# Performance work log

Hardware: AMD Instinct MI355X
Metric: run time of the kernel (lower is better)

The kernel has to match this reference:

```python
import jax, jax.numpy as jnp
import numpy as np

N0, N1, N2 = 16000, 12000, 6000
K0, K1 = 10, 5
H, OUT = 256, 128
VOCABS = [50000, 1000, 200]
EDIMS = [64, 32, 32]
EIN = sum(EDIMS)  # 128 input to fc_input


def setup_inputs() -> dict:
    key = jax.random.key(0)
    ks = jax.random.split(key, 40)
    inp = {}
    cols = [jax.random.randint(ks[i], (N0, 1), 0, VOCABS[i]) for i in range(3)]
    inp['x'] = jnp.concatenate(cols, axis=1)
    inp['idx_sim0'] = jax.random.randint(ks[3], (N1, K0), 0, N0)
    inp['idx_cor0'] = jax.random.randint(ks[4], (N1, K0), 0, N0)
    inp['idx_sim1'] = jax.random.randint(ks[5], (N2, K1), 0, N1)
    inp['idx_cor1'] = jax.random.randint(ks[6], (N2, K1), 0, N1)
    k = 7
    for m in ['sim', 'cor']:
        for i in range(3):
            inp[f'emb{i}_{m}'] = jax.random.normal(ks[k], (VOCABS[i], EDIMS[i]), jnp.float32) * 0.02; k += 1
        inp[f'Win_{m}'] = jax.random.normal(ks[k], (EIN, H), jnp.float32) * (1.0 / np.sqrt(EIN)); k += 1
        inp[f'bin_{m}'] = jnp.zeros((H,), jnp.float32)
        inp[f'Wout_{m}'] = jax.random.normal(ks[k], (H, OUT), jnp.float32) * (1.0 / np.sqrt(H)); k += 1
        inp[f'bout_{m}'] = jnp.zeros((OUT,), jnp.float32)
    inp['Ws2c'] = jax.random.normal(ks[k], (OUT, OUT), jnp.float32) * (1.0 / np.sqrt(OUT)); k += 1
    inp['Wc2s'] = jax.random.normal(ks[k], (OUT, OUT), jnp.float32) * (1.0 / np.sqrt(OUT)); k += 1
    inp['a1'] = jnp.array([0.3], jnp.float32)
    inp['a2'] = jnp.array([0.25], jnp.float32)
    inp['b2'] = jnp.array([0.2], jnp.float32)
    return inp


def _coattention(D, Q):
    # D, Q: [N, K, H]
    L = jnp.einsum('nkh,nmh->nkm', D, Q)          # [N, K, K]
    AC = jax.nn.softmax(L, axis=-1)
    AS = jax.nn.softmax(jnp.swapaxes(L, 1, 2), axis=-1)
    CQ = jnp.einsum('nkm,nmh->nkh', AC, Q)        # [N, K, H]
    CD = jnp.einsum('nkm,nmh->nkh', AS, jnp.concatenate([D, CQ], axis=-1))  # [N, K, 2H]
    return jnp.concatenate([Q, CD], axis=-1)       # [N, K, 3H]


def _coagg(feat, idx_sim, idx_cor, mode, n_dst):
    # gather neighbor features per dst node (feat_src[in_edges_id])
    if mode == 'cor':
        D, Q = feat[idx_sim], feat[idx_cor]
    else:
        D, Q = feat[idx_cor], feat[idx_sim]
    h = _coattention(D, Q)                         # [n_dst, K, 3H]
    n, k, f = h.shape
    # AvgPool1d(kernel=3, stride=3) over feature axis -> [n_dst, K, H]
    pooled = h.reshape(n, k, f // 3, 3).mean(axis=-1)
    neigh = pooled.mean(axis=1)                    # mean over neighbors -> [n_dst, H]
    return feat[:n_dst] + neigh


def _branch(x, e0, e1, e2, Win, bin_, Wout, bout, i_s0, i_c0, i_s1, i_c1, mode):
    e = jnp.concatenate([e0[x[:, 0]], e1[x[:, 1]], e2[x[:, 2]]], axis=1)  # [N0, 128]
    h = e @ Win + bin_                             # [N0, H]
    h = jax.nn.relu(_coagg(h, i_s0, i_c0, mode, N1))
    h = _coagg(h, i_s1, i_c1, mode, N2)
    return h @ Wout + bout                         # [N2, OUT]


def reference(x, idx_sim0, idx_cor0, idx_sim1, idx_cor1,
              emb0_sim, emb1_sim, emb2_sim, Win_sim, bin_sim, Wout_sim, bout_sim,
              emb0_cor, emb1_cor, emb2_cor, Win_cor, bin_cor, Wout_cor, bout_cor,
              Ws2c, Wc2s, a1, a2, b2):
    sim = _branch(x, emb0_sim, emb1_sim, emb2_sim, Win_sim, bin_sim, Wout_sim, bout_sim,
                  idx_sim0, idx_cor0, idx_sim1, idx_cor1, 'sim')
    cor = _branch(x, emb0_cor, emb1_cor, emb2_cor, Win_cor, bin_cor, Wout_cor, bout_cor,
                  idx_sim0, idx_cor0, idx_sim1, idx_cor1, 'cor')
    # SemanticIntegration
    z1sim = (1 - a1) * sim + a1 * (cor @ Wc2s)
    z1cor = (1 - a1) * cor + a1 * (sim @ Ws2c)
    z2sim = (1 - a2 - b2) * sim + a2 * (cor @ Wc2s) + b2 * (z1cor @ Wc2s)
    z2cor = (1 - a2 - b2) * cor + a2 * (sim @ Ws2c) + b2 * (z1sim @ Ws2c)
    return jnp.stack([z2sim, z2cor])               # [2, N2, OUT]
```

## Files before the change

kernel.cpp:

```cpp
#include <hip/hip_runtime.h>

#define CH 256

template <int CTRL>
__device__ __forceinline__ float dppAdd(float v) {
    const int m = __builtin_amdgcn_update_dpp(0, __builtin_bit_cast(int, v), CTRL, 0xf, 0xf, true);
    return v + __builtin_bit_cast(float, m);
}

#define OPAQUE4(v) asm volatile("" : "+v"((v).x), "+v"((v).y), "+v"((v).z), "+v"((v).w))

__device__ __forceinline__ unsigned short f2bf(float f) {
    unsigned int x = __builtin_bit_cast(unsigned int, f);
    return (unsigned short)((x + 0x7fffu + ((x >> 16) & 1u)) >> 16);
}
__device__ __forceinline__ float bf2f(unsigned short u) {
    return __builtin_bit_cast(float, ((unsigned int)u) << 16);
}

__global__ __launch_bounds__(256) void embed_fc2_kernel(
    const int* __restrict__ x,
    const float* __restrict__ e0a, const float* __restrict__ e1a, const float* __restrict__ e2a,
    const float* __restrict__ Wina, const float* __restrict__ bina, unsigned short* __restrict__ h0a,
    const float* __restrict__ e0b, const float* __restrict__ e1b, const float* __restrict__ e2b,
    const float* __restrict__ Winb, const float* __restrict__ binb, unsigned short* __restrict__ h0b,
    const int blocksPer)
{
    __shared__ __align__(16) float eT[128][32];
    int bid = blockIdx.x;
    const float *e0, *e1, *e2, *Win, *bin;
    unsigned short* h0;
    if (bid < blocksPer) { e0 = e0a; e1 = e1a; e2 = e2a; Win = Wina; bin = bina; h0 = h0a; }
    else { bid -= blocksPer; e0 = e0b; e1 = e1b; e2 = e2b; Win = Winb; bin = binb; h0 = h0b; }

    const int row0 = bid * 32;
    const int t = threadIdx.x;
    const int w = t >> 6, l = t & 63;
    const int r = l & 31;
    const int kcBase = 2 * w + (l >> 5);

#pragma unroll
    for (int j = 0; j < 4; ++j) {
        const int kc = kcBase + 8 * j;
        const int k0 = kc * 4;
        const int row = row0 + r;
        float4 v;
        if (kc < 16)      v = *(const float4*)(e0 + (size_t)x[row * 3 + 0] * 64 + k0);
        else if (kc < 24) v = *(const float4*)(e1 + (size_t)x[row * 3 + 1] * 32 + (k0 - 64));
        else              v = *(const float4*)(e2 + (size_t)x[row * 3 + 2] * 32 + (k0 - 96));
        eT[k0 + 0][r] = v.x; eT[k0 + 1][r] = v.y; eT[k0 + 2][r] = v.z; eT[k0 + 3][r] = v.w;
    }
    __syncthreads();

    const float4 bb = *(const float4*)(bin + l * 4);
    float acc[8][4];
#pragma unroll
    for (int rr = 0; rr < 8; ++rr) {
        acc[rr][0] = bb.x; acc[rr][1] = bb.y; acc[rr][2] = bb.z; acc[rr][3] = bb.w;
    }
#pragma unroll 4
    for (int k = 0; k < 128; ++k) {
        const float4 wv = *(const float4*)(Win + (size_t)k * 256 + l * 4);
        const float4 ea = *(const float4*)&eT[k][w * 8];
        const float4 eb = *(const float4*)&eT[k][w * 8 + 4];
        const float ev[8] = {ea.x, ea.y, ea.z, ea.w, eb.x, eb.y, eb.z, eb.w};
#pragma unroll
        for (int rr = 0; rr < 8; ++rr) {
            acc[rr][0] += ev[rr] * wv.x; acc[rr][1] += ev[rr] * wv.y;
            acc[rr][2] += ev[rr] * wv.z; acc[rr][3] += ev[rr] * wv.w;
        }
    }
#pragma unroll
    for (int rr = 0; rr < 8; ++rr) {
        ushort4 o;
        o.x = f2bf(acc[rr][0]); o.y = f2bf(acc[rr][1]);
        o.z = f2bf(acc[rr][2]); o.w = f2bf(acc[rr][3]);
        *(ushort4*)(h0 + (size_t)(row0 + w * 8 + rr) * 256 + l * 4) = o;
    }
}

template <int KD, int MODE>
__global__ __launch_bounds__(128) void gemm16_kernel(
    const float* __restrict__ ina, const float* __restrict__ Wa,
    const float* __restrict__ auxa, const float* __restrict__ aux2a, float* __restrict__ oa,
    const float* __restrict__ inb, const float* __restrict__ Wb,
    const float* __restrict__ auxb, const float* __restrict__ aux2b, float* __restrict__ ob,
    const int blocksPer, const int nRows,
    const float* __restrict__ a1p, const float* __restrict__ a2p, const float* __restrict__ b2p)
{
    __shared__ __align__(16) float inT[KD][16];
    int bid = blockIdx.x;
    const float *in, *W, *aux, *aux2; float* outp;
    if (bid < blocksPer) { in = ina; W = Wa; aux = auxa; aux2 = aux2a; outp = oa; }
    else { bid -= blocksPer; in = inb; W = Wb; aux = auxb; aux2 = aux2b; outp = ob; }

    const int row0 = bid * 16;
    const int t = threadIdx.x;
    const int row = t & 15;
    const int kc0 = t >> 4;

#pragma unroll
    for (int j = 0; j < KD / 32; ++j) {
        const int kc = kc0 + 8 * j;
        const int k0 = kc * 4;
        int r = row0 + row;
        if (r >= nRows) r = nRows - 1;
        const float4 v = *(const float4*)(in + (size_t)r * KD + k0);
        inT[k0 + 0][row] = v.x; inT[k0 + 1][row] = v.y;
        inT[k0 + 2][row] = v.z; inT[k0 + 3][row] = v.w;
    }
    __syncthreads();

    const int w = t >> 6, l = t & 63;
    const int rg = w * 2 + (l >> 5);
    const int r0 = rg * 4;
    const int cc0 = (l & 31) * 4;

    float acc[4][4];
    if constexpr (MODE == 0) {
        const float4 bb = *(const float4*)(aux + cc0);
#pragma unroll
        for (int rr = 0; rr < 4; ++rr) {
            acc[rr][0] = bb.x; acc[rr][1] = bb.y; acc[rr][2] = bb.z; acc[rr][3] = bb.w;
        }
    } else {
#pragma unroll
        for (int rr = 0; rr < 4; ++rr) acc[rr][0] = acc[rr][1] = acc[rr][2] = acc[rr][3] = 0.f;
    }

#pragma unroll 4
    for (int k = 0; k < KD; ++k) {
        const float4 wv = *(const float4*)(W + (size_t)k * 128 + cc0);
        const float4 ea = *(const float4*)&inT[k][r0];
        const float ev[4] = {ea.x, ea.y, ea.z, ea.w};
#pragma unroll
        for (int rr = 0; rr < 4; ++rr) {
            acc[rr][0] += ev[rr] * wv.x; acc[rr][1] += ev[rr] * wv.y;
            acc[rr][2] += ev[rr] * wv.z; acc[rr][3] += ev[rr] * wv.w;
        }
    }

    float c0 = 0.f, c1 = 0.f, c2 = 0.f;
    if constexpr (MODE == 1) {
        const float a1 = *a1p, a2 = *a2p, b2 = *b2p;
        c0 = 1.f - a2 - b2;
        c1 = a2 + b2 * (1.f - a1);
        c2 = b2 * a1;
    }

#pragma unroll
    for (int rr = 0; rr < 4; ++rr) {
        const int r = row0 + r0 + rr;
        if (r < nRows) {
            float4 o = make_float4(acc[rr][0], acc[rr][1], acc[rr][2], acc[rr][3]);
            if constexpr (MODE == 1) {
                const size_t idx = (size_t)r * 128 + cc0;
                const float4 b1v = *(const float4*)(aux + idx);
                const float4 b2v = *(const float4*)(aux2 + idx);
                o.x = c0 * b1v.x + c1 * b2v.x + c2 * o.x;
                o.y = c0 * b1v.y + c1 * b2v.y + c2 * o.y;
                o.z = c0 * b1v.z + c1 * b2v.z + c2 * o.z;
                o.w = c0 * b1v.w + c1 * b2v.w + c2 * o.w;
            }
            *(float4*)(outp + (size_t)r * 128 + cc0) = o;
        }
    }
}

template <int K, bool BF16IN>
__global__ __launch_bounds__(256, 2) void coagg_kernel(
    const void* __restrict__ fa, const int* __restrict__ iDa, const int* __restrict__ iQa,
    float* __restrict__ oa,
    const void* __restrict__ fb, const int* __restrict__ iDb, const int* __restrict__ iQb,
    float* __restrict__ ob,
    const int nPer, const int relu)
{
    __shared__ float sL[4][K][K];
    __shared__ float sAC[4][K][K];
    __shared__ float sAS[4][K][K];
    __shared__ float sw_[4][K], su_[4][K];
    __shared__ __align__(16) float sHsum[4][768];

    const int t = threadIdx.x;
    const int wv = t >> 6, lane = t & 63;
    int n = blockIdx.x * 4 + wv;

    const void* feat; const int* idxD; const int* idxQ; float* outp;
    if (n < nPer) { feat = fa; idxD = iDa; idxQ = iQa; outp = oa; }
    else { n -= nPer; feat = fb; idxD = iDb; idxQ = iQb; outp = ob; }

    float4 d[K], q[K], resid;
    if constexpr (BF16IN) {
        const unsigned short* fpu = (const unsigned short*)feat;
#pragma unroll
        for (int k = 0; k < K; ++k) {
            const int rD = idxD[n * K + k];
            const int rQ = idxQ[n * K + k];
            const ushort4 ud = *(const ushort4*)(fpu + (size_t)rD * 256 + lane * 4);
            const ushort4 uq = *(const ushort4*)(fpu + (size_t)rQ * 256 + lane * 4);
            d[k] = make_float4(bf2f(ud.x), bf2f(ud.y), bf2f(ud.z), bf2f(ud.w));
            q[k] = make_float4(bf2f(uq.x), bf2f(uq.y), bf2f(uq.z), bf2f(uq.w));
        }
        const ushort4 ur = *(const ushort4*)(fpu + (size_t)n * 256 + lane * 4);
        resid = make_float4(bf2f(ur.x), bf2f(ur.y), bf2f(ur.z), bf2f(ur.w));
    } else {
        const float4* fp = (const float4*)feat;
#pragma unroll
        for (int k = 0; k < K; ++k) {
            const int rD = idxD[n * K + k];
            const int rQ = idxQ[n * K + k];
            d[k] = fp[(size_t)rD * 64 + lane];
            q[k] = fp[(size_t)rQ * 64 + lane];
        }
        resid = fp[(size_t)n * 64 + lane];
    }
#pragma unroll
    for (int k = 0; k < K; ++k) { OPAQUE4(d[k]); OPAQUE4(q[k]); }

#pragma unroll
    for (int k = 0; k < K; ++k) {
        const float4 dd = d[k];
#pragma unroll
        for (int m0 = 0; m0 < K; m0 += 4) {
            const float4 q0 = q[m0];
            float s0 = dd.x * q0.x + dd.y * q0.y + dd.z * q0.z + dd.w * q0.w;
            float s1 = 0.f, s2 = 0.f, s3 = 0.f;
            if (m0 + 1 < K) {
                const float4 qq = q[(m0 + 1 < K) ? m0 + 1 : 0];
                s1 = dd.x * qq.x + dd.y * qq.y + dd.z * qq.z + dd.w * qq.w;
            }
            if (m0 + 2 < K) {
                const float4 qq = q[(m0 + 2 < K) ? m0 + 2 : 0];
                s2 = dd.x * qq.x + dd.y * qq.y + dd.z * qq.z + dd.w * qq.w;
            }
            if (m0 + 3 < K) {
                const float4 qq = q[(m0 + 3 < K) ? m0 + 3 : 0];
                s3 = dd.x * qq.x + dd.y * qq.y + dd.z * qq.z + dd.w * qq.w;
            }
            asm volatile("v_permlane32_swap_b32 %0, %1" : "+v"(s0), "+v"(s1));
            float a = s0 + s1;
            asm volatile("v_permlane32_swap_b32 %0, %1" : "+v"(s2), "+v"(s3));
            float b = s2 + s3;
            asm volatile("v_permlane16_swap_b32 %0, %1" : "+v"(a), "+v"(b));
            float r = a + b;
            r = dppAdd<0x111>(r);
            r = dppAdd<0x112>(r);
            r = dppAdd<0x114>(r);
            r = dppAdd<0x118>(r);
            const int rowid = lane >> 4;
            const int mm = m0 + (((rowid & 1) << 1) | (rowid >> 1));
            if ((lane & 15) == 15 && mm < K) sL[wv][k][mm] = r;
        }
    }

    if (lane < K) {
        float e_[K], mx = -1e30f;
#pragma unroll
        for (int m = 0; m < K; ++m) mx = fmaxf(mx, sL[wv][lane][m]);
        float ssum = 0.f;
#pragma unroll
        for (int m = 0; m < K; ++m) { e_[m] = __expf(sL[wv][lane][m] - mx); ssum += e_[m]; }
        const float inv = 1.f / ssum;
#pragma unroll
        for (int m = 0; m < K; ++m) sAC[wv][lane][m] = e_[m] * inv;
    }
    {
        const int c = lane - 16;
        if (c >= 0 && c < K) {
            float e_[K], mx = -1e30f;
#pragma unroll
            for (int m = 0; m < K; ++m) mx = fmaxf(mx, sL[wv][m][c]);
            float ssum = 0.f;
#pragma unroll
            for (int m = 0; m < K; ++m) { e_[m] = __expf(sL[wv][m][c] - mx); ssum += e_[m]; }
            const float inv = 1.f / ssum;
#pragma unroll
            for (int m = 0; m < K; ++m) sAS[wv][c][m] = e_[m] * inv;
        }
    }
    {
        const int m2 = lane - 32;
        if (m2 >= 0 && m2 < K) {
            float s = 0.f;
#pragma unroll
            for (int k2 = 0; k2 < K; ++k2) s += sAS[wv][k2][m2];
            sw_[wv][m2] = s;
        }
    }
    {
        const int j2 = lane - 48;
        if (j2 >= 0 && j2 < K) {
            float s = 0.f;
#pragma unroll
            for (int m = 0; m < K; ++m) s += sw_[wv][m] * sAC[wv][m][j2];
            su_[wv][j2] = s;
        }
    }

    float4 h0v = make_float4(0.f, 0.f, 0.f, 0.f);
    float4 h1v = make_float4(0.f, 0.f, 0.f, 0.f);
    float4 h2v = make_float4(0.f, 0.f, 0.f, 0.f);
#pragma unroll
    for (int kx = 0; kx < K; ++kx) {
        const float wk = sw_[wv][kx];
        const float uk = su_[wv][kx];
        const float4 qq = q[kx];
        const float4 dd = d[kx];
        h0v.x += qq.x;      h0v.y += qq.y;      h0v.z += qq.z;      h0v.w += qq.w;
        h1v.x += wk * dd.x; h1v.y += wk * dd.y; h1v.z += wk * dd.z; h1v.w += wk * dd.w;
        h2v.x += uk * qq.x; h2v.y += uk * qq.y; h2v.z += uk * qq.z; h2v.w += uk * qq.w;
    }
    ((float4*)&sHsum[wv][0])[lane]       = h0v;
    ((float4*)&sHsum[wv][0])[64 + lane]  = h1v;
    ((float4*)&sHsum[wv][0])[128 + lane] = h2v;

    float ov[4];
#pragma unroll
    for (int i = 0; i < 4; ++i) {
        const int f = lane * 4 + i;
        ov[i] = (sHsum[wv][3 * f] + sHsum[wv][3 * f + 1] + sHsum[wv][3 * f + 2])
                * (1.0f / (3.0f * K));
    }
    float4 o = make_float4(resid.x + ov[0], resid.y + ov[1],
                           resid.z + ov[2], resid.w + ov[3]);
    if (relu) {
        o.x = fmaxf(o.x, 0.f); o.y = fmaxf(o.y, 0.f);
        o.z = fmaxf(o.z, 0.f); o.w = fmaxf(o.w, 0.f);
    }
    ((float4*)outp)[(size_t)n * 64 + lane] = o;
}

extern "C" void kernel_launch(void* const* d_in, const int* in_sizes, int n_in,
                              void* d_out, int out_size, void* d_ws, size_t ws_size,
                              hipStream_t stream)
{
    const int* x        = (const int*)d_in[0];
    const int* idx_sim0 = (const int*)d_in[1];
    const int* idx_cor0 = (const int*)d_in[2];
    const int* idx_sim1 = (const int*)d_in[3];
    const int* idx_cor1 = (const int*)d_in[4];
    const float* e0s  = (const float*)d_in[5];
    const float* e1s  = (const float*)d_in[6];
    const float* e2s  = (const float*)d_in[7];
    const float* Wins = (const float*)d_in[8];
    const float* bins = (const float*)d_in[9];
    const float* Wouts= (const float*)d_in[10];
    const float* bouts= (const float*)d_in[11];
    const float* e0c  = (const float*)d_in[12];
    const float* e1c  = (const float*)d_in[13];
    const float* e2c  = (const float*)d_in[14];
    const float* Winc = (const float*)d_in[15];
    const float* binc = (const float*)d_in[16];
    const float* Woutc= (const float*)d_in[17];
    const float* boutc= (const float*)d_in[18];
    const float* Ws2c = (const float*)d_in[19];
    const float* Wc2s = (const float*)d_in[20];
    const float* a1 = (const float*)d_in[21];
    const float* a2 = (const float*)d_in[22];
    const float* b2 = (const float*)d_in[23];

    float* outSim = (float*)d_out;
    float* outCor = outSim + 6000 * 128;

    float* ws = (float*)d_ws;
    const size_t needMerged = (size_t)(2 * 16000 * 256 + 2 * 12000 * 256 + 2 * 6000 * 256 + 4 * 6000 * 128) * 4;
    const bool merged = ws_size >= needMerged;

    const int fcBlocks = 6000 / 16;

    if (merged) {
        unsigned short* A0 = (unsigned short*)ws;
        unsigned short* A1 = (unsigned short*)(ws + 16000 * 256);
        float* B0 = ws + 2 * 16000 * 256;
        float* B1 = B0 + 12000 * 256;
        float* C0 = B1 + 12000 * 256;
        float* C1 = C0 + 6000 * 256;
        float* simO = C1 + 6000 * 256;
        float* corO = simO + 6000 * 128;
        float* P    = corO + 6000 * 128;
        float* S    = P + 6000 * 128;

        embed_fc2_kernel<<<1000, 256, 0, stream>>>(x,
            e0s, e1s, e2s, Wins, bins, A0,
            e0c, e1c, e2c, Winc, binc, A1, 500);
        coagg_kernel<10, true><<<6000, 256, 0, stream>>>(
            A0, idx_cor0, idx_sim0, B0,
            A1, idx_sim0, idx_cor0, B1, 12000, 1);
        coagg_kernel<5, false><<<3000, 256, 0, stream>>>(
            B0, idx_cor1, idx_sim1, C0,
            B1, idx_sim1, idx_cor1, C1, 6000, 0);
        gemm16_kernel<256, 0><<<2 * fcBlocks, 128, 0, stream>>>(
            C0, Wouts, bouts, nullptr, simO,
            C1, Woutc, boutc, nullptr, corO, fcBlocks, 6000, a1, a2, b2);
        gemm16_kernel<128, 2><<<2 * fcBlocks, 128, 0, stream>>>(
            corO, Wc2s, nullptr, nullptr, P,
            simO, Ws2c, nullptr, nullptr, S, fcBlocks, 6000, a1, a2, b2);
        gemm16_kernel<128, 1><<<2 * fcBlocks, 128, 0, stream>>>(
            S, Wc2s, simO, P, outSim,
            P, Ws2c, corO, S, outCor, fcBlocks, 6000, a1, a2, b2);
    } else {
        unsigned short* A = (unsigned short*)ws;
        float* B = ws + 16000 * 256;
        float* C = B + 12000 * 256;
        float* simO = C + 6000 * 256;
        float* corO = simO + 6000 * 128;
        float* P    = corO + 6000 * 128;
        float* S    = P + 6000 * 128;

        for (int b = 0; b < 2; ++b) {
            const float* e0   = (b == 0) ? e0s : e0c;
            const float* e1   = (b == 0) ? e1s : e1c;
            const float* e2   = (b == 0) ? e2s : e2c;
            const float* Win  = (b == 0) ? Wins : Winc;
            const float* bin  = (b == 0) ? bins : binc;
            const float* Wout = (b == 0) ? Wouts : Woutc;
            const float* bout = (b == 0) ? bouts : boutc;
            const int* iD0 = (b == 0) ? idx_cor0 : idx_sim0;
            const int* iQ0 = (b == 0) ? idx_sim0 : idx_cor0;
            const int* iD1 = (b == 0) ? idx_cor1 : idx_sim1;
            const int* iQ1 = (b == 0) ? idx_sim1 : idx_cor1;
            float* branchOut = (b == 0) ? simO : corO;

            embed_fc2_kernel<<<500, 256, 0, stream>>>(x,
                e0, e1, e2, Win, bin, A,
                e0, e1, e2, Win, bin, A, 500);
            coagg_kernel<10, true><<<3000, 256, 0, stream>>>(
                A, iD0, iQ0, B, A, iD0, iQ0, B, 12000, 1);
            coagg_kernel<5, false><<<1500, 256, 0, stream>>>(
                B, iD1, iQ1, C, B, iD1, iQ1, C, 6000, 0);
            gemm16_kernel<256, 0><<<fcBlocks, 128, 0, stream>>>(
                C, Wout, bout, nullptr, branchOut,
                C, Wout, bout, nullptr, branchOut, fcBlocks, 6000, a1, a2, b2);
        }
        gemm16_kernel<128, 2><<<2 * fcBlocks, 128, 0, stream>>>(
            corO, Wc2s, nullptr, nullptr, P,
            simO, Ws2c, nullptr, nullptr, S, fcBlocks, 6000, a1, a2, b2);
        gemm16_kernel<128, 1><<<2 * fcBlocks, 128, 0, stream>>>(
            S, Wc2s, simO, P, outSim,
            P, Ws2c, corO, S, outCor, fcBlocks, 6000, a1, a2, b2);
    }
}
```

Before: 157.2 us.

## Store layer-1 coagg output in bf16 and fuse integration GEMMs into one kernel

The first coattention layer now writes its intermediate features as bf16, and the second layer reads them as bf16. This halves the bytes moved through the gather-heavy second stage. The two semantic-integration GEMM launches are merged into one kernel that keeps the intermediate S/P products in shared memory, which removes one launch and a global round trip. In exchange, the layer-1 output loses precision, and the fused kernel uses small 8-row tiles that reread the weight matrices many times.

```diff
diff --git a/kernel.cpp b/kernel.cpp
--- a/kernel.cpp
+++ b/kernel.cpp
@@ -79,20 +79,18 @@
     }
 }
 
-template <int KD, int MODE>
-__global__ __launch_bounds__(128) void gemm16_kernel(
+__global__ __launch_bounds__(128) void fcout_kernel(
     const float* __restrict__ ina, const float* __restrict__ Wa,
-    const float* __restrict__ auxa, const float* __restrict__ aux2a, float* __restrict__ oa,
+    const float* __restrict__ auxa, float* __restrict__ oa,
     const float* __restrict__ inb, const float* __restrict__ Wb,
-    const float* __restrict__ auxb, const float* __restrict__ aux2b, float* __restrict__ ob,
-    const int blocksPer, const int nRows,
-    const float* __restrict__ a1p, const float* __restrict__ a2p, const float* __restrict__ b2p)
+    const float* __restrict__ auxb, float* __restrict__ ob,
+    const int blocksPer, const int nRows)
 {
-    __shared__ __align__(16) float inT[KD][16];
+    __shared__ __align__(16) float inT[256][16];
     int bid = blockIdx.x;
-    const float *in, *W, *aux, *aux2; float* outp;
-    if (bid < blocksPer) { in = ina; W = Wa; aux = auxa; aux2 = aux2a; outp = oa; }
-    else { bid -= blocksPer; in = inb; W = Wb; aux = auxb; aux2 = aux2b; outp = ob; }
+    const float *in, *W, *aux; float* outp;
+    if (bid < blocksPer) { in = ina; W = Wa; aux = auxa; outp = oa; }
+    else { bid -= blocksPer; in = inb; W = Wb; aux = auxb; outp = ob; }
 
     const int row0 = bid * 16;
     const int t = threadIdx.x;
@@ -100,12 +98,12 @@
     const int kc0 = t >> 4;
 
 #pragma unroll
-    for (int j = 0; j < KD / 32; ++j) {
+    for (int j = 0; j < 8; ++j) {
         const int kc = kc0 + 8 * j;
         const int k0 = kc * 4;
         int r = row0 + row;
         if (r >= nRows) r = nRows - 1;
-        const float4 v = *(const float4*)(in + (size_t)r * KD + k0);
+        const float4 v = *(const float4*)(in + (size_t)r * 256 + k0);
         inT[k0 + 0][row] = v.x; inT[k0 + 1][row] = v.y;
         inT[k0 + 2][row] = v.z; inT[k0 + 3][row] = v.w;
     }
@@ -117,19 +115,14 @@
     const int cc0 = (l & 31) * 4;
 
     float acc[4][4];
-    if constexpr (MODE == 0) {
-        const float4 bb = *(const float4*)(aux + cc0);
-#pragma unroll
-        for (int rr = 0; rr < 4; ++rr) {
-            acc[rr][0] = bb.x; acc[rr][1] = bb.y; acc[rr][2] = bb.z; acc[rr][3] = bb.w;
-        }
-    } else {
-#pragma unroll
-        for (int rr = 0; rr < 4; ++rr) acc[rr][0] = acc[rr][1] = acc[rr][2] = acc[rr][3] = 0.f;
+    const float4 bb = *(const float4*)(aux + cc0);
+#pragma unroll
+    for (int rr = 0; rr < 4; ++rr) {
+        acc[rr][0] = bb.x; acc[rr][1] = bb.y; acc[rr][2] = bb.z; acc[rr][3] = bb.w;
     }
 
 #pragma unroll 4
-    for (int k = 0; k < KD; ++k) {
+    for (int k = 0; k < 256; ++k) {
         const float4 wv = *(const float4*)(W + (size_t)k * 128 + cc0);
         const float4 ea = *(const float4*)&inT[k][r0];
         const float ev[4] = {ea.x, ea.y, ea.z, ea.w};
@@ -140,39 +133,92 @@
         }
     }
 
-    float c0 = 0.f, c1 = 0.f, c2 = 0.f;
-    if constexpr (MODE == 1) {
-        const float a1 = *a1p, a2 = *a2p, b2 = *b2p;
-        c0 = 1.f - a2 - b2;
-        c1 = a2 + b2 * (1.f - a1);
-        c2 = b2 * a1;
-    }
-
 #pragma unroll
     for (int rr = 0; rr < 4; ++rr) {
         const int r = row0 + r0 + rr;
         if (r < nRows) {
-            float4 o = make_float4(acc[rr][0], acc[rr][1], acc[rr][2], acc[rr][3]);
-            if constexpr (MODE == 1) {
-                const size_t idx = (size_t)r * 128 + cc0;
-                const float4 b1v = *(const float4*)(aux + idx);
-                const float4 b2v = *(const float4*)(aux2 + idx);
-                o.x = c0 * b1v.x + c1 * b2v.x + c2 * o.x;
-                o.y = c0 * b1v.y + c1 * b2v.y + c2 * o.y;
-                o.z = c0 * b1v.z + c1 * b2v.z + c2 * o.z;
-                o.w = c0 * b1v.w + c1 * b2v.w + c2 * o.w;
-            }
-            *(float4*)(outp + (size_t)r * 128 + cc0) = o;
-        }
-    }
-}
-
-template <int K, bool BF16IN>
+            *(float4*)(outp + (size_t)r * 128 + cc0) =
+                make_float4(acc[rr][0], acc[rr][1], acc[rr][2], acc[rr][3]);
+        }
+    }
+}
+
+__global__ __launch_bounds__(256) void integ_fused_kernel(
+    const float* __restrict__ simO, const float* __restrict__ corO,
+    const float* __restrict__ Ws2c, const float* __restrict__ Wc2s,
+    const float* __restrict__ a1p, const float* __restrict__ a2p,
+    const float* __restrict__ b2p,
+    float* __restrict__ outSim, float* __restrict__ outCor)
+{
+    __shared__ float sT[128][9], cT[128][9], ST[128][9], PT[128][9];
+    const int t = threadIdx.x;
+    const int row0 = blockIdx.x * 8;
+
+    {
+        const int row = t & 7;
+        const int k0 = (t >> 3) * 4;
+        float4 v = *(const float4*)(simO + (size_t)(row0 + row) * 128 + k0);
+        sT[k0 + 0][row] = v.x; sT[k0 + 1][row] = v.y;
+        sT[k0 + 2][row] = v.z; sT[k0 + 3][row] = v.w;
+        v = *(const float4*)(corO + (size_t)(row0 + row) * 128 + k0);
+        cT[k0 + 0][row] = v.x; cT[k0 + 1][row] = v.y;
+        cT[k0 + 2][row] = v.z; cT[k0 + 3][row] = v.w;
+    }
+    __syncthreads();
+
+    const int w = t >> 6, l = t & 63;
+    const int r0 = w * 2 + (l >> 5);
+    const int cc0 = (l & 31) * 4;
+
+    float S[4] = {0.f, 0.f, 0.f, 0.f}, P[4] = {0.f, 0.f, 0.f, 0.f};
+#pragma unroll 4
+    for (int k = 0; k < 128; ++k) {
+        const float4 wS = *(const float4*)(Ws2c + (size_t)k * 128 + cc0);
+        const float4 wC = *(const float4*)(Wc2s + (size_t)k * 128 + cc0);
+        const float eS = sT[k][r0];
+        const float eC = cT[k][r0];
+        S[0] += eS * wS.x; S[1] += eS * wS.y; S[2] += eS * wS.z; S[3] += eS * wS.w;
+        P[0] += eC * wC.x; P[1] += eC * wC.y; P[2] += eC * wC.z; P[3] += eC * wC.w;
+    }
+#pragma unroll
+    for (int i = 0; i < 4; ++i) { ST[cc0 + i][r0] = S[i]; PT[cc0 + i][r0] = P[i]; }
+    __syncthreads();
+
+    float T1[4] = {0.f, 0.f, 0.f, 0.f}, T2[4] = {0.f, 0.f, 0.f, 0.f};
+#pragma unroll 4
+    for (int k = 0; k < 128; ++k) {
+        const float4 wC = *(const float4*)(Wc2s + (size_t)k * 128 + cc0);
+        const float4 wS = *(const float4*)(Ws2c + (size_t)k * 128 + cc0);
+        const float eS2 = ST[k][r0];
+        const float eP  = PT[k][r0];
+        T1[0] += eS2 * wC.x; T1[1] += eS2 * wC.y; T1[2] += eS2 * wC.z; T1[3] += eS2 * wC.w;
+        T2[0] += eP * wS.x;  T2[1] += eP * wS.y;  T2[2] += eP * wS.z;  T2[3] += eP * wS.w;
+    }
+
+    const float a1 = *a1p, a2 = *a2p, b2 = *b2p;
+    const float c0 = 1.f - a2 - b2;
+    const float c1 = a2 + b2 * (1.f - a1);
+    const float c2 = b2 * a1;
+    float4 oS, oC;
+    oS.x = c0 * sT[cc0 + 0][r0] + c1 * P[0] + c2 * T1[0];
+    oS.y = c0 * sT[cc0 + 1][r0] + c1 * P[1] + c2 * T1[1];
+    oS.z = c0 * sT[cc0 + 2][r0] + c1 * P[2] + c2 * T1[2];
+    oS.w = c0 * sT[cc0 + 3][r0] + c1 * P[3] + c2 * T1[3];
+    oC.x = c0 * cT[cc0 + 0][r0] + c1 * S[0] + c2 * T2[0];
+    oC.y = c0 * cT[cc0 + 1][r0] + c1 * S[1] + c2 * T2[1];
+    oC.z = c0 * cT[cc0 + 2][r0] + c1 * S[2] + c2 * T2[2];
+    oC.w = c0 * cT[cc0 + 3][r0] + c1 * S[3] + c2 * T2[3];
+    const size_t idx = (size_t)(row0 + r0) * 128 + cc0;
+    *(float4*)(outSim + idx) = oS;
+    *(float4*)(outCor + idx) = oC;
+}
+
+template <int K, bool BF16IN, bool BF16OUT>
 __global__ __launch_bounds__(256, 2) void coagg_kernel(
     const void* __restrict__ fa, const int* __restrict__ iDa, const int* __restrict__ iQa,
-    float* __restrict__ oa,
+    void* __restrict__ oa,
     const void* __restrict__ fb, const int* __restrict__ iDb, const int* __restrict__ iQb,
-    float* __restrict__ ob,
+    void* __restrict__ ob,
     const int nPer, const int relu)
 {
     __shared__ float sL[4][K][K];
@@ -185,7 +231,7 @@
     const int wv = t >> 6, lane = t & 63;
     int n = blockIdx.x * 4 + wv;
 
-    const void* feat; const int* idxD; const int* idxQ; float* outp;
+    const void* feat; const int* idxD; const int* idxQ; void* outp;
     if (n < nPer) { feat = fa; idxD = iDa; idxQ = iQa; outp = oa; }
     else { n -= nPer; feat = fb; idxD = iDb; idxQ = iQb; outp = ob; }
 
@@ -327,7 +373,13 @@
         o.x = fmaxf(o.x, 0.f); o.y = fmaxf(o.y, 0.f);
         o.z = fmaxf(o.z, 0.f); o.w = fmaxf(o.w, 0.f);
     }
-    ((float4*)outp)[(size_t)n * 64 + lane] = o;
+    if constexpr (BF16OUT) {
+        ushort4 ou;
+        ou.x = f2bf(o.x); ou.y = f2bf(o.y); ou.z = f2bf(o.z); ou.w = f2bf(o.w);
+        *(ushort4*)((unsigned short*)outp + (size_t)n * 256 + lane * 4) = ou;
+    } else {
+        ((float4*)outp)[(size_t)n * 64 + lane] = o;
+    }
 }
 
 extern "C" void kernel_launch(void* const* d_in, const int* in_sizes, int n_in,
@@ -371,41 +423,33 @@
     if (merged) {
         unsigned short* A0 = (unsigned short*)ws;
         unsigned short* A1 = (unsigned short*)(ws + 16000 * 256);
-        float* B0 = ws + 2 * 16000 * 256;
-        float* B1 = B0 + 12000 * 256;
-        float* C0 = B1 + 12000 * 256;
+        unsigned short* B0 = (unsigned short*)(ws + 2 * 16000 * 256);
+        unsigned short* B1 = (unsigned short*)(ws + 2 * 16000 * 256 + 12000 * 256);
+        float* C0 = ws + 2 * 16000 * 256 + 2 * 12000 * 256;
         float* C1 = C0 + 6000 * 256;
         float* simO = C1 + 6000 * 256;
         float* corO = simO + 6000 * 128;
-        float* P    = corO + 6000 * 128;
-        float* S    = P + 6000 * 128;
 
         embed_fc2_kernel<<<1000, 256, 0, stream>>>(x,
             e0s, e1s, e2s, Wins, bins, A0,
             e0c, e1c, e2c, Winc, binc, A1, 500);
-        coagg_kernel<10, true><<<6000, 256, 0, stream>>>(
+        coagg_kernel<10, true, true><<<6000, 256, 0, stream>>>(
             A0, idx_cor0, idx_sim0, B0,
             A1, idx_sim0, idx_cor0, B1, 12000, 1);
-        coagg_kernel<5, false><<<3000, 256, 0, stream>>>(
+        coagg_kernel<5, true, false><<<3000, 256, 0, stream>>>(
             B0, idx_cor1, idx_sim1, C0,
             B1, idx_sim1, idx_cor1, C1, 6000, 0);
-        gemm16_kernel<256, 0><<<2 * fcBlocks, 128, 0, stream>>>(
-            C0, Wouts, bouts, nullptr, simO,
-            C1, Woutc, boutc, nullptr, corO, fcBlocks, 6000, a1, a2, b2);
-        gemm16_kernel<128, 2><<<2 * fcBlocks, 128, 0, stream>>>(
-            corO, Wc2s, nullptr, nullptr, P,
-            simO, Ws2c, nullptr, nullptr, S, fcBlocks, 6000, a1, a2, b2);
-        gemm16_kernel<128, 1><<<2 * fcBlocks, 128, 0, stream>>>(
-            S, Wc2s, simO, P, outSim,
-            P, Ws2c, corO, S, outCor, fcBlocks, 6000, a1, a2, b2);
+        fcout_kernel<<<2 * fcBlocks, 128, 0, stream>>>(
+            C0, Wouts, bouts, simO,
+            C1, Woutc, boutc, corO, fcBlocks, 6000);
+        integ_fused_kernel<<<750, 256, 0, stream>>>(
+            simO, corO, Ws2c, Wc2s, a1, a2, b2, outSim, outCor);
     } else {
         unsigned short* A = (unsigned short*)ws;
-        float* B = ws + 16000 * 256;
-        float* C = B + 12000 * 256;
+        unsigned short* B = (unsigned short*)(ws + 16000 * 256);
+        float* C = ws + 16000 * 256 + 12000 * 256;
         float* simO = C + 6000 * 256;
         float* corO = simO + 6000 * 128;
-        float* P    = corO + 6000 * 128;
-        float* S    = P + 6000 * 128;
 
         for (int b = 0; b < 2; ++b) {
             const float* e0   = (b == 0) ? e0s : e0c;
@@ -424,19 +468,15 @@
             embed_fc2_kernel<<<500, 256, 0, stream>>>(x,
                 e0, e1, e2, Win, bin, A,
                 e0, e1, e2, Win, bin, A, 500);
-            coagg_kernel<10, true><<<3000, 256, 0, stream>>>(
+            coagg_kernel<10, true, true><<<3000, 256, 0, stream>>>(
                 A, iD0, iQ0, B, A, iD0, iQ0, B, 12000, 1);
-            coagg_kernel<5, false><<<1500, 256, 0, stream>>>(
+            coagg_kernel<5, true, false><<<1500, 256, 0, stream>>>(
                 B, iD1, iQ1, C, B, iD1, iQ1, C, 6000, 0);
-            gemm16_kernel<256, 0><<<fcBlocks, 128, 0, stream>>>(
-                C, Wout, bout, nullptr, branchOut,
-                C, Wout, bout, nullptr, branchOut, fcBlocks, 6000, a1, a2, b2);
-        }
-        gemm16_kernel<128, 2><<<2 * fcBlocks, 128, 0, stream>>>(
-            corO, Wc2s, nullptr, nullptr, P,
-            simO, Ws2c, nullptr, nullptr, S, fcBlocks, 6000, a1, a2, b2);
-        gemm16_kernel<128, 1><<<2 * fcBlocks, 128, 0, stream>>>(
-            S, Wc2s, simO, P, outSim,
-            P, Ws2c, corO, S, outCor, fcBlocks, 6000, a1, a2, b2);
-    }
-}
+            fcout_kernel<<<fcBlocks, 128, 0, stream>>>(
+                C, Wout, bout, branchOut,
+                C, Wout, bout, branchOut, fcBlocks, 6000);
+        }
+        integ_fused_kernel<<<750, 256, 0, stream>>>(
+            simO, corO, Ws2c, Wc2s, a1, a2, b2, outSim, outCor);
+    }
+}
```

After: 175.3 us. 11.5% more time.
